# Performance work log

Hardware: AMD Instinct MI355X
Metric: run time of the kernel (lower is better)

The kernel has to match this reference:

```python
import jax, jax.numpy as jnp
import numpy as np

BATCH, LENGTH, DIM, CHANNEL, PAST = 16, 256, 512, 8, 12


def setup_inputs() -> dict:
    key = jax.random.key(0)
    ks = jax.random.split(key, 5)
    scale = 1.0 / np.sqrt(DIM)
    inp = jax.random.normal(ks[0], (BATCH, LENGTH, DIM), dtype=jnp.float32)
    Ws = jax.random.normal(ks[1], (CHANNEL, DIM, DIM), dtype=jnp.float32) * scale
    bs = jax.random.normal(ks[2], (CHANNEL, DIM), dtype=jnp.float32) * scale
    Wt = jax.random.normal(ks[3], (CHANNEL, PAST), dtype=jnp.float32) * (1.0 / np.sqrt(PAST))
    bt = jax.random.normal(ks[4], (CHANNEL,), dtype=jnp.float32) * 0.01
    return {"inp": inp, "Ws": Ws, "bs": bs, "Wt": Wt, "bt": bt, "past": PAST}


def reference(inp, Ws, bs, Wt, bt, past):
    # Per-channel spatial linear: y = x @ Ws[c].T + bs[c]
    # spat: [batch, length, channel, dim]
    spat = jnp.einsum('bld,cod->blco', inp, Ws) + bs[None, None, :, :]
    Lout = inp.shape[1] - past
    # Causal sliding-window temporal linear (depthwise conv over time):
    # out[b,t,c,d] = sum_p Wt[c,p] * spat[b,t+p,c,d] + bt[c]
    out = bt[None, None, :, None]
    for p in range(past):  # small fixed loop over kernel taps
        out = out + Wt[:, p][None, None, :, None] * spat[:, p:p + Lout]
    return out  # [batch, length-past, channel, dim]
```

## Files before the change

### kernel.cpp

```cpp
#include <hip/hip_runtime.h>
#include <hip/hip_bf16.h>

#define B_   16
#define L_   256
#define D_   512
#define C_   8
#define P_   12
#define LOUT 244
#define O_   512
#define GM   3904
#define BM   128
#define BN   256
#define BK   32
#define NMT  31
#define NNT  2
#define NSTEP 16
#define NFIRB 488

typedef __attribute__((ext_vector_type(8))) short bf16x8;
typedef __attribute__((ext_vector_type(4))) float f32x4;

__device__ __forceinline__ unsigned short f2bf(float f) {
    unsigned int u = __float_as_uint(f);
    unsigned int r = (u + 0x7FFFu + ((u >> 16) & 1u)) >> 16;
    return (unsigned short)r;
}

__device__ __forceinline__ void async_copy16(const void* g, void* l) {
    __builtin_amdgcn_global_load_lds(
        (const __attribute__((address_space(1))) unsigned int*)g,
        (__attribute__((address_space(3))) unsigned int*)l, 16, 0, 0);
}

__global__ __launch_bounds__(256) void prep(const float* __restrict__ inp,
                                            const float* __restrict__ Ws,
                                            const float* __restrict__ Wt,
                                            unsigned short* __restrict__ tmp,
                                            unsigned short* __restrict__ wsb) {
    int bid = blockIdx.x;
    int tid = threadIdx.x;

    if (bid >= NFIRB) {
        int g = (bid - NFIRB) * 256 + tid;
        float4 v = ((const float4*)Ws)[g];
        ushort4 o;
        o.x = f2bf(v.x); o.y = f2bf(v.y); o.z = f2bf(v.z); o.w = f2bf(v.w);
        ((ushort4*)wsb)[g] = o;
        return;
    }

    __shared__ float wt_s[C_][P_];
    if (tid < C_ * P_) wt_s[tid / P_][tid % P_] = Wt[tid];
    __syncthreads();

    int task = bid * 2 + (tid >> 7);
    int dq   = tid & 127;
    int b  = task / 61, lg = task % 61;
    int l0 = lg * 4;
    int d0 = dq * 4;

    float4 rv[15];
    const float* ibase = inp + ((size_t)b * L_ + l0) * D_ + d0;
#pragma unroll
    for (int j = 0; j < 15; ++j)
        rv[j] = *(const float4*)(ibase + (size_t)j * D_);

#pragma unroll
    for (int c = 0; c < C_; ++c) {
        float w[P_];
#pragma unroll
        for (int p = 0; p < P_; ++p) w[p] = wt_s[c][p];
        unsigned short* ob = tmp + (((size_t)(c * B_ + b)) * LOUT + l0) * D_ + d0;
#pragma unroll
        for (int j = 0; j < 4; ++j) {
            float sx = 0.f, sy = 0.f, sz = 0.f, sw = 0.f;
#pragma unroll
            for (int p = 0; p < P_; ++p) {
                sx += w[p] * rv[j + p].x;
                sy += w[p] * rv[j + p].y;
                sz += w[p] * rv[j + p].z;
                sw += w[p] * rv[j + p].w;
            }
            ushort4 ov;
            ov.x = f2bf(sx); ov.y = f2bf(sy);
            ov.z = f2bf(sz); ov.w = f2bf(sw);
            *(ushort4*)(ob + (size_t)j * D_) = ov;
        }
    }
}

__global__ __launch_bounds__(512, 4) void gemm_k(const unsigned short* __restrict__ tmp,
                                                 const unsigned short* __restrict__ wsb,
                                                 const float* __restrict__ bs,
                                                 const float* __restrict__ Wt,
                                                 const float* __restrict__ bt,
                                                 float* __restrict__ out) {
    __shared__ unsigned short As[3][BM * BK];
    __shared__ unsigned short Bs[3][BN * BK];

    int bid = blockIdx.x;
    int c  = bid & 7;
    int t2 = bid >> 3;
    int nt = t2 & 1;
    int mt = t2 >> 1;
    int row0 = mt * BM;
    int o0   = nt * BN;
    int tid = threadIdx.x, lane = tid & 63, wid = tid >> 6;
    int wm = wid >> 2, wn = wid & 3;

    const unsigned short* Ab = tmp + (size_t)c * GM * D_;
    const unsigned short* Bb = wsb + ((size_t)c * O_ + o0) * D_;

    f32x4 acc[4][4];
#pragma unroll
    for (int m = 0; m < 4; ++m)
#pragma unroll
        for (int n = 0; n < 4; ++n)
            acc[m][n] = (f32x4){0.f, 0.f, 0.f, 0.f};

#define STAGE(bi, kb)                                                         \
    {                                                                         \
        int qa = tid;                                                         \
        int rowa = qa >> 2, cca = qa & 3;                                     \
        int sca = cca ^ (rowa & 3);                                           \
        int ar = row0 + rowa; if (ar > GM - 1) ar = GM - 1;                   \
        async_copy16(Ab + (size_t)ar * D_ + (kb) + sca * 8,                   \
                     (unsigned short*)As[bi] + qa * 8);                       \
        _Pragma("unroll")                                                     \
        for (int h = 0; h < 2; ++h) {                                         \
            int q = h * 512 + tid;                                            \
            int row = q >> 2, cc = q & 3;                                     \
            int sc = cc ^ (row & 3);                                          \
            async_copy16(Bb + (size_t)row * D_ + (kb) + sc * 8,               \
                         (unsigned short*)Bs[bi] + q * 8);                    \
        }                                                                     \
    }

#define MFMA_STEP(bi)                                                         \
    {                                                                         \
        bf16x8 af[4], bq[4];                                                  \
        _Pragma("unroll")                                                     \
        for (int m = 0; m < 4; ++m) {                                         \
            int r = wm * 64 + m * 16 + (lane & 15);                           \
            af[m] = *(const bf16x8*)&As[bi][r * BK +                          \
                    (((lane >> 4) ^ (r & 3)) << 3)];                          \
        }                                                                     \
        _Pragma("unroll")                                                     \
        for (int n = 0; n < 4; ++n) {                                         \
            int o = wn * 64 + n * 16 + (lane & 15);                           \
            bq[n] = *(const bf16x8*)&Bs[bi][o * BK +                          \
                    (((lane >> 4) ^ (o & 3)) << 3)];                          \
        }                                                                     \
        _Pragma("unroll")                                                     \
        for (int m = 0; m < 4; ++m)                                           \
            _Pragma("unroll")                                                 \
            for (int n = 0; n < 4; ++n)                                       \
                acc[m][n] = __builtin_amdgcn_mfma_f32_16x16x32_bf16(          \
                    af[m], bq[n], acc[m][n], 0, 0, 0);                        \
    }

    STAGE(0, 0)
    STAGE(1, BK)
    asm volatile("s_waitcnt vmcnt(0)" ::: "memory");
    __builtin_amdgcn_sched_barrier(0);
    asm volatile("s_barrier" ::: "memory");

#pragma unroll
    for (int t = 0; t < NSTEP; ++t) {
        MFMA_STEP(t % 3)
        if (t == NSTEP - 1) break;
        asm volatile("s_waitcnt lgkmcnt(0)" ::: "memory");
        __builtin_amdgcn_sched_barrier(0);
        if (t + 2 < NSTEP) STAGE((t + 2) % 3, (t + 2) * BK)
        if (t < NSTEP - 2)
            asm volatile("s_waitcnt vmcnt(3)" ::: "memory");
        else
            asm volatile("s_waitcnt vmcnt(0)" ::: "memory");
        __builtin_amdgcn_sched_barrier(0);
        asm volatile("s_barrier" ::: "memory");
    }

    float S = 0.f;
#pragma unroll
    for (int p = 0; p < P_; ++p) S += Wt[c * P_ + p];
    float btc = bt[c];

#pragma unroll
    for (int m = 0; m < 4; ++m) {
        int rb = row0 + wm * 64 + m * 16 + ((lane >> 4) << 2);
#pragma unroll
        for (int n = 0; n < 4; ++n) {
            int col = o0 + wn * 64 + n * 16 + (lane & 15);
            float add = bs[c * O_ + col] * S + btc;
#pragma unroll
            for (int i = 0; i < 4; ++i) {
                int r = rb + i;
                if (r < GM)
                    out[((size_t)r * C_ + c) * O_ + col] = acc[m][n][i] + add;
            }
        }
    }
#undef STAGE
#undef MFMA_STEP
}

__global__ __launch_bounds__(256) void naive_k(const float* __restrict__ inp,
                                               const float* __restrict__ Ws,
                                               const float* __restrict__ bs,
                                               const float* __restrict__ Wt,
                                               const float* __restrict__ bt,
                                               float* __restrict__ out) {
    __shared__ float tmp[D_];
    int bid = blockIdx.x;
    int c = bid & 7; int r = bid >> 3;
    int l = r % LOUT; int b = r / LOUT;
    int tid = threadIdx.x;

    for (int d = tid; d < D_; d += 256) {
        float s = 0.f;
        for (int p = 0; p < P_; ++p)
            s += Wt[c * P_ + p] * inp[((size_t)b * L_ + l + p) * D_ + d];
        tmp[d] = s;
    }
    __syncthreads();
    float S = 0.f;
    for (int p = 0; p < P_; ++p) S += Wt[c * P_ + p];
    for (int o = tid; o < O_; o += 256) {
        const float* wrow = Ws + ((size_t)c * O_ + o) * D_;
        float s = 0.f;
        for (int d = 0; d < D_; ++d) s += wrow[d] * tmp[d];
        out[(((size_t)b * LOUT + l) * C_ + c) * O_ + o] =
            s + bs[c * O_ + o] * S + bt[c];
    }
}

extern "C" void kernel_launch(void* const* d_in, const int* in_sizes, int n_in,
                              void* d_out, int out_size, void* d_ws, size_t ws_size,
                              hipStream_t stream) {
    const float* inp = (const float*)d_in[0];
    const float* Ws  = (const float*)d_in[1];
    const float* bs  = (const float*)d_in[2];
    const float* Wt  = (const float*)d_in[3];
    const float* bt  = (const float*)d_in[4];
    float* out = (float*)d_out;

    const size_t TMPB = (size_t)C_ * GM * D_ * 2;
    const size_t WSBB = (size_t)C_ * O_ * D_ * 2;

    if (ws_size >= TMPB + WSBB) {
        unsigned short* tmpb = (unsigned short*)d_ws;
        unsigned short* wsb  = (unsigned short*)((char*)d_ws + TMPB);
        prep<<<NFIRB + 2048, 256, 0, stream>>>(inp, Ws, Wt, tmpb, wsb);
        gemm_k<<<NMT * NNT * C_, 512, 0, stream>>>(tmpb, wsb, bs, Wt, bt, out);
    } else {
        naive_k<<<B_ * LOUT * C_, 256, 0, stream>>>(inp, Ws, bs, Wt, bt, out);
    }
}
```

Before: 41.43 us.

## Stage GEMM epilogue through LDS for float4 stores and split FIR prep across channel groups

The GEMM epilogue now writes each warp's accumulator tile to a padded LDS scratch area (reusing the B staging buffer after a barrier). It then reads the tile back row-wise so each lane emits coalesced float4 global stores with a vectorized bias add, replacing scattered scalar stores. The prep kernel also doubles its FIR block count: each block handles one (batch, length-group) task and its two thread halves split the eight channels. This raises parallelism but means input rows are loaded twice. The epilogue adds an extra barrier and LDS round trips.

```diff
diff --git a/kernel.cpp b/kernel.cpp
--- a/kernel.cpp
+++ b/kernel.cpp
@@ -15,7 +15,7 @@
 #define NMT  31
 #define NNT  2
 #define NSTEP 16
-#define NFIRB 488
+#define NFIRB 976
 
 typedef __attribute__((ext_vector_type(8))) short bf16x8;
 typedef __attribute__((ext_vector_type(4))) float f32x4;
@@ -53,9 +53,9 @@
     if (tid < C_ * P_) wt_s[tid / P_][tid % P_] = Wt[tid];
     __syncthreads();
 
-    int task = bid * 2 + (tid >> 7);
-    int dq   = tid & 127;
-    int b  = task / 61, lg = task % 61;
+    int b = bid / 61, lg = bid % 61;
+    int cg = tid >> 7;
+    int dq = tid & 127;
     int l0 = lg * 4;
     int d0 = dq * 4;
 
@@ -66,7 +66,8 @@
         rv[j] = *(const float4*)(ibase + (size_t)j * D_);
 
 #pragma unroll
-    for (int c = 0; c < C_; ++c) {
+    for (int cc = 0; cc < 4; ++cc) {
+        int c = cg * 4 + cc;
         float w[P_];
 #pragma unroll
         for (int p = 0; p < P_; ++p) w[p] = wt_s[c][p];
@@ -180,23 +181,41 @@
         asm volatile("s_barrier" ::: "memory");
     }
 
+    asm volatile("s_waitcnt lgkmcnt(0)" ::: "memory");
+    __builtin_amdgcn_sched_barrier(0);
+    asm volatile("s_barrier" ::: "memory");
+
     float S = 0.f;
 #pragma unroll
     for (int p = 0; p < P_; ++p) S += Wt[c * P_ + p];
     float btc = bt[c];
 
+    float* scr = (float*)&Bs[0][0] + wid * (16 * 68);
+    int colg = o0 + wn * 64 + (lane & 15) * 4;
+    float4 bs4 = *(const float4*)&bs[c * O_ + colg];
+    float4 addv;
+    addv.x = bs4.x * S + btc; addv.y = bs4.y * S + btc;
+    addv.z = bs4.z * S + btc; addv.w = bs4.w * S + btc;
+
 #pragma unroll
     for (int m = 0; m < 4; ++m) {
-        int rb = row0 + wm * 64 + m * 16 + ((lane >> 4) << 2);
-#pragma unroll
-        for (int n = 0; n < 4; ++n) {
-            int col = o0 + wn * 64 + n * 16 + (lane & 15);
-            float add = bs[c * O_ + col] * S + btc;
-#pragma unroll
-            for (int i = 0; i < 4; ++i) {
-                int r = rb + i;
-                if (r < GM)
-                    out[((size_t)r * C_ + c) * O_ + col] = acc[m][n][i] + add;
+#pragma unroll
+        for (int n = 0; n < 4; ++n)
+#pragma unroll
+            for (int i = 0; i < 4; ++i)
+                scr[((lane >> 4) * 4 + i) * 68 + n * 16 + (lane & 15)] =
+                    acc[m][n][i];
+        int gr0 = row0 + wm * 64 + m * 16;
+#pragma unroll
+        for (int rp = 0; rp < 4; ++rp) {
+            int lrow = rp * 4 + (lane >> 4);
+            float4 v = *(float4*)&scr[lrow * 68 + (lane & 15) * 4];
+            int grow = gr0 + lrow;
+            if (grow < GM) {
+                float4 o4;
+                o4.x = v.x + addv.x; o4.y = v.y + addv.y;
+                o4.z = v.z + addv.z; o4.w = v.w + addv.w;
+                *(float4*)&out[((size_t)grow * C_ + c) * O_ + colg] = o4;
             }
         }
     }
```

After: 41.96 us. Within noise of the previous version (+1.3%).
